# Optimization experiments

Measured on AMD Instinct MI355X. Metric: run time of the kernel, lower is better.

The kernel has to match this reference:

```python
import math
import jax, jax.numpy as jnp
import numpy as np

ALPHA = 0.2                         # LeakyReLU slope
LAMBDA_INIT = 0.8 - 0.6 * math.exp(-0.3 * 1)  # lambda_init_fn(depth=1)
NEG_INF = -9e15
EPS_LN = 1e-5

B, N, IN_F, OUT_F = 4, 2048, 512, 512
INTERNAL = OUT_F // 2
REL_DIM = 10
NUM_REL = 6


def setup_inputs() -> dict:
    key = jax.random.key(0)
    ks = jax.random.split(key, 16)
    xav = lambda k, shape, fan: jax.random.normal(k, shape, jnp.float32) * (1.414 * math.sqrt(2.0 / fan))
    h = jax.random.normal(ks[0], (B, N, IN_F), jnp.float32)
    adj = jax.random.randint(ks[1], (B, N, N), 0, NUM_REL, jnp.int32)
    W = xav(ks[2], (IN_F, OUT_F), IN_F + OUT_F)
    a_left_pos = xav(ks[3], (INTERNAL,), INTERNAL + 1)
    a_right_pos = xav(ks[4], (INTERNAL,), INTERNAL + 1)
    a_left_neg = xav(ks[5], (INTERNAL,), INTERNAL + 1)
    a_right_neg = xav(ks[6], (INTERNAL,), INTERNAL + 1)
    rel_table = jax.random.normal(ks[7], (NUM_REL, REL_DIM), jnp.float32)
    a_rel_pos = xav(ks[8], (REL_DIM,), REL_DIM + 1)
    a_rel_neg = xav(ks[9], (REL_DIM,), REL_DIM + 1)
    ll1 = 0.1 * jax.random.normal(ks[10], (INTERNAL,), jnp.float32)
    lr1 = 0.1 * jax.random.normal(ks[11], (INTERNAL,), jnp.float32)
    ll2 = 0.1 * jax.random.normal(ks[12], (INTERNAL,), jnp.float32)
    lr2 = 0.1 * jax.random.normal(ks[13], (INTERNAL,), jnp.float32)
    ln_gamma = jnp.ones((OUT_F,), jnp.float32)
    ln_beta = jnp.zeros((OUT_F,), jnp.float32)
    return dict(h=h, adj=adj, W=W, a_left_pos=a_left_pos, a_right_pos=a_right_pos,
                a_left_neg=a_left_neg, a_right_neg=a_right_neg, rel_table=rel_table,
                a_rel_pos=a_rel_pos, a_rel_neg=a_rel_neg, ll1=ll1, lr1=lr1,
                ll2=ll2, lr2=lr2, ln_gamma=ln_gamma, ln_beta=ln_beta)


def _leaky(x):
    return jnp.where(x >= 0, x, ALPHA * x)


def reference(h, adj, W, a_left_pos, a_right_pos, a_left_neg, a_right_neg,
              rel_table, a_rel_pos, a_rel_neg, ll1, lr1, ll2, lr2,
              ln_gamma, ln_beta):
    # Projection: Wh [B,N,out] -> split into pos/neg halves [B,N,internal]
    Wh = jnp.einsum('bni,io->bno', h, W)
    Bn, Nn, _ = Wh.shape
    Wh2 = Wh.reshape(Bn, Nn, 2, INTERNAL)
    Wh_pos, Wh_neg = Wh2[:, :, 0, :], Wh2[:, :, 1, :]

    # Additive GAT-style scores: e[b,i,j] = a_left.Wh[i] + a_right.Wh[j]
    e_pos = (Wh_pos @ a_left_pos)[:, :, None] + (Wh_pos @ a_right_pos)[:, None, :]
    e_neg = (Wh_neg @ a_left_neg)[:, :, None] + (Wh_neg @ a_right_neg)[:, None, :]

    # Relation-embedding bias: gather [B,N,N,rel_dim] then project to scalar
    rel_emb = rel_table[adj]                       # [B,N,N,R]
    e_pos = e_pos + rel_emb @ a_rel_pos
    e_neg = e_neg + rel_emb @ a_rel_neg

    mask = adj > 0
    att_pos = jax.nn.softmax(jnp.where(mask, _leaky(e_pos), NEG_INF), axis=2)
    att_neg = jax.nn.softmax(jnp.where(mask, _leaky(e_neg), NEG_INF), axis=2)

    lam = jnp.exp(jnp.sum(ll1 * lr1)) - jnp.exp(jnp.sum(ll2 * lr2)) + LAMBDA_INIT
    attention = att_pos - lam * att_neg            # dropout is identity (eval)

    Wh_v = jnp.concatenate([Wh_pos, Wh_neg], axis=-1)   # [B,N,out]
    h_prime = jnp.einsum('bij,bjd->bid', attention, Wh_v)

    mu = jnp.mean(h_prime, axis=-1, keepdims=True)
    var = jnp.mean(jnp.square(h_prime - mu), axis=-1, keepdims=True)
    h_prime = (h_prime - mu) / jnp.sqrt(var + EPS_LN) * ln_gamma + ln_beta
    h_prime = h_prime * (1 - LAMBDA_INIT)
    return jax.nn.gelu(h_prime, approximate=False), attention
```

## Files before the change

kernel.cpp:

```cpp
#include <hip/hip_runtime.h>
#include <hip/hip_bf16.h>


#define B_ 4
#define N_ 2048
#define F_ 512
#define ALPHA_ 0.2f
#define NEG_INF_ -9000000000000000.0f
#define EPS_LN_ 1e-5f

typedef __attribute__((ext_vector_type(8))) short bf16x8;
typedef __attribute__((ext_vector_type(4))) short bf16x4;
typedef __attribute__((ext_vector_type(4))) float f32x4;

#define HBF_OFF   0
#define WT_OFF    8388608
#define EL_OFF    8912896
#define HP_OFF    0
#define WHT_OFF   16777216
#define ATTBF_OFF 25165824
#define CANON_OFF 58720256
#define SC_OFF    58724352
#define V_OFF     58724416

__device__ __forceinline__ float bf_as_f32(unsigned short u) {
    return __uint_as_float(((unsigned)u) << 16);
}
__device__ __forceinline__ float ldf(const void* p, long i, int isf32) {
    return isf32 ? ((const float*)p)[i] : bf_as_f32(((const unsigned short*)p)[i]);
}
__device__ __forceinline__ short f2bf(float f) {
    __hip_bfloat16 t = __float2bfloat16(f);
    return *reinterpret_cast<short*>(&t);
}
__device__ __forceinline__ int detect_f32(const unsigned short* p) {
    float mx = 0.f;
    for (int i = 0; i < 64; ++i) {
        float x = fabsf(bf_as_f32(p[i]));
        if (x == x && x > mx) mx = x;
    }
    return mx > 1e10f;
}

#define GLL16(g, l) __builtin_amdgcn_global_load_lds( \
    (const __attribute__((address_space(1))) void*)(g), \
    (__attribute__((address_space(3))) void*)(l), 16, 0, 0)

__global__ __launch_bounds__(256) void k_pre(const unsigned short* __restrict__ hraw, const void* __restrict__ W,
                                             const void* alp, const void* arp, const void* aln, const void* arn,
                                             const void* rel, const void* arelp, const void* areln,
                                             const void* ll1, const void* lr1, const void* ll2, const void* lr2,
                                             const void* gam, const void* bet,
                                             __hip_bfloat16* __restrict__ Wt, float* __restrict__ v,
                                             float* __restrict__ canon, float* __restrict__ sc) {
    __shared__ float t[32][33];
    int fl = detect_f32(hraw);
    int bi = blockIdx.x, tid = threadIdx.x, lane = tid & 63, wid = tid >> 6;
    if (bi < 256) {
        int k0 = (bi & 15) * 32, o0 = (bi >> 4) * 32;
        int tx = tid & 31, ty = tid >> 5;
#pragma unroll
        for (int r = 0; r < 4; ++r)
            t[ty + r * 8][tx] = ldf(W, (long)(k0 + ty + r * 8) * 512 + o0 + tx, fl);
        __syncthreads();
#pragma unroll
        for (int r = 0; r < 4; ++r)
            Wt[(o0 + ty + r * 8) * 512 + k0 + tx] = __float2bfloat16(t[tx][ty + r * 8]);
    } else if (bi < 272) {
        int k = (bi - 256) * 32 + (tid >> 3);
        int seg = tid & 7;
        int pos = seg < 4;
        int ob = (seg & 3) * 64 + (pos ? 0 : 256);
        const void* aL = pos ? alp : aln;
        const void* aR = pos ? arp : arn;
        float sL = 0.f, sR = 0.f;
        for (int e = 0; e < 64; ++e) {
            float w = ldf(W, (long)k * 512 + ob + e, fl);
            sL += w * ldf(aL, (ob & 255) + e, fl);
            sR += w * ldf(aR, (ob & 255) + e, fl);
        }
        sL += __shfl_xor(sL, 1); sL += __shfl_xor(sL, 2);
        sR += __shfl_xor(sR, 1); sR += __shfl_xor(sR, 2);
        if ((seg & 3) == 0) {
            int vb = pos ? 0 : 2;
            v[vb * 512 + k] = sL;
            v[(vb + 1) * 512 + k] = sR;
        }
    } else {
        canon[tid] = ldf(gam, tid, fl);
        canon[256 + tid] = ldf(gam, 256 + tid, fl);
        canon[512 + tid] = ldf(bet, tid, fl);
        canon[768 + tid] = ldf(bet, 256 + tid, fl);
        if (wid == 0) {
            float s1 = 0.f, s2 = 0.f;
            for (int k = lane; k < 256; k += 64) {
                s1 += ldf(ll1, k, fl) * ldf(lr1, k, fl);
                s2 += ldf(ll2, k, fl) * ldf(lr2, k, fl);
            }
            for (int off = 32; off; off >>= 1) { s1 += __shfl_down(s1, off); s2 += __shfl_down(s2, off); }
            if (lane == 0) {
                float lam_init = 0.8f - 0.6f * expf(-0.3f);
                sc[0] = expf(s1) - expf(s2) + lam_init;
            }
        } else if (wid == 1 && lane < 6) {
            float p = 0.f, n = 0.f;
            for (int d = 0; d < 10; ++d) {
                float rv = ldf(rel, lane * 10 + d, fl);
                p += rv * ldf(arelp, d, fl);
                n += rv * ldf(areln, d, fl);
            }
            sc[1 + lane] = p;
            sc[7 + lane] = n;
        }
    }
}

__global__ __launch_bounds__(256) void k_conv(const void* __restrict__ h, short* __restrict__ hbf,
                                              const float* __restrict__ v, float* __restrict__ el) {
    int fl = detect_f32((const unsigned short*)h);
    int tid = threadIdx.x, lane = tid & 63;
    long i = ((long)blockIdx.x * 256 + tid) * 8;
    int row = (int)(i >> 9);
    float f[8];
    if (fl) {
        const float4* p = (const float4*)((const float*)h + i);
        float4 a = p[0], b = p[1];
        f[0] = a.x; f[1] = a.y; f[2] = a.z; f[3] = a.w;
        f[4] = b.x; f[5] = b.y; f[6] = b.z; f[7] = b.w;
    } else {
        bf16x8 x = *(const bf16x8*)((const short*)h + i);
#pragma unroll
        for (int e = 0; e < 8; ++e) f[e] = bf_as_f32((unsigned short)x[e]);
    }
    bf16x8 vv;
#pragma unroll
    for (int e = 0; e < 8; ++e) vv[e] = f2bf(f[e]);
    *(bf16x8*)(hbf + i) = vv;
    const float* v0 = v + 0 * 512 + lane * 8;
    const float* v1 = v + 1 * 512 + lane * 8;
    const float* v2 = v + 2 * 512 + lane * 8;
    const float* v3 = v + 3 * 512 + lane * 8;
    float slp = 0.f, srp = 0.f, sln = 0.f, srn = 0.f;
#pragma unroll
    for (int e = 0; e < 8; ++e) {
        slp += f[e] * v0[e]; srp += f[e] * v1[e];
        sln += f[e] * v2[e]; srn += f[e] * v3[e];
    }
    for (int off = 32; off; off >>= 1) {
        slp += __shfl_xor(slp, off); srp += __shfl_xor(srp, off);
        sln += __shfl_xor(sln, off); srn += __shfl_xor(srn, off);
    }
    if (lane == 0) {
        el[row] = slp; el[8192 + row] = srp; el[16384 + row] = sln; el[24576 + row] = srn;
    }
}

template<int TRANS_OUT>
__global__ __launch_bounds__(256) void k_gemm(const short* __restrict__ A, const short* __restrict__ B,
                                              void* __restrict__ Cout, int K, int N,
                                              long aBatch, long bBatch, long cBatch) {
    __shared__ short SM[24576];
    short* As = SM;
    short* Bs = SM + 16384;
    int tid = threadIdx.x, wid = tid >> 6, lane = tid & 63;
    int bm = blockIdx.x * 128, bn = blockIdx.y * 64, bz = blockIdx.z;
    const short* Ab = A + bz * aBatch + (long)bm * K;
    const short* Bb = B + bz * bBatch + (long)bn * K;
    f32x4 acc[4][2] = {};
    int wr = (wid >> 1) * 64, wc = (wid & 1) * 32;
    int l15 = lane & 15, lhi = lane >> 4;
    for (int k0 = 0; k0 < K; k0 += 128) {
        __syncthreads();
#pragma unroll
        for (int j = 0; j < 8; ++j) {
            int q = tid + j * 256;
            int row = q >> 4, c = (q & 15) ^ (row & 7);
            GLL16(Ab + (long)row * K + k0 + c * 8, As + q * 8);
        }
#pragma unroll
        for (int j = 0; j < 4; ++j) {
            int q = tid + j * 256;
            int row = q >> 4, c = (q & 15) ^ (row & 7);
            GLL16(Bb + (long)row * K + k0 + c * 8, Bs + q * 8);
        }
        __syncthreads();
#pragma unroll
        for (int ks = 0; ks < 4; ++ks) {
            bf16x8 af[4], bq[2];
#pragma unroll
            for (int m = 0; m < 4; ++m) {
                int r = wr + m * 16 + l15;
                int c = (ks * 4 + lhi) ^ (r & 7);
                af[m] = *(const bf16x8*)&As[r * 128 + c * 8];
            }
#pragma unroll
            for (int n = 0; n < 2; ++n) {
                int r = wc + n * 16 + l15;
                int c = (ks * 4 + lhi) ^ (r & 7);
                bq[n] = *(const bf16x8*)&Bs[r * 128 + c * 8];
            }
#pragma unroll
            for (int m = 0; m < 4; ++m)
#pragma unroll
                for (int n = 0; n < 2; ++n)
                    acc[m][n] = __builtin_amdgcn_mfma_f32_16x16x32_bf16(af[m], bq[n], acc[m][n], 0, 0, 0);
        }
    }
    int rg = lhi * 4;
    if (TRANS_OUT == 0) {
        float* C = (float*)Cout + bz * cBatch;
#pragma unroll
        for (int m = 0; m < 4; ++m)
#pragma unroll
            for (int n = 0; n < 2; ++n)
#pragma unroll
                for (int r = 0; r < 4; ++r)
                    C[(long)(bm + wr + m * 16 + rg + r) * N + bn + wc + n * 16 + l15] = acc[m][n][r];
    } else {
        __syncthreads();
        short* T = SM;
#pragma unroll
        for (int m = 0; m < 4; ++m)
#pragma unroll
            for (int n = 0; n < 2; ++n) {
                bf16x4 p;
#pragma unroll
                for (int r = 0; r < 4; ++r) p[r] = f2bf(acc[m][n][r]);
                int o = wc + n * 16 + l15;
                int jj = wr + m * 16 + rg;
                *(bf16x4*)&T[o * 136 + jj] = p;
            }
        __syncthreads();
        int b = bm >> 11, jb = bm & 2047;
        int o = tid >> 2, sg = tid & 3;
        short* Wg = (short*)Cout + ((long)b * 512 + bn + o) * 2048 + jb + sg * 32;
#pragma unroll
        for (int w2 = 0; w2 < 4; ++w2)
            *(bf16x8*)(Wg + w2 * 8) = *(bf16x8*)&T[o * 136 + sg * 32 + w2 * 8];
    }
}

__global__ __launch_bounds__(256) void k_attn(const int* __restrict__ adj,
                                              const float* __restrict__ el, const float* __restrict__ sc,
                                              float* __restrict__ att_f32,
                                              __hip_bfloat16* __restrict__ att_bf) {
    __shared__ float s_rp[8], s_rn[8], s_lam[1];
    __shared__ float rmp[4], rmn[4], rsp[4], rsn[4];
    int tid = threadIdx.x, lane = tid & 63, wid = tid >> 6;
    if (tid < 6) { s_rp[tid] = sc[1 + tid]; s_rn[tid] = sc[7 + tid]; }
    if (tid == 6) s_lam[0] = sc[0];
    int m = blockIdx.x, b = m >> 11;
    float elp = el[m], eln = el[16384 + m];
    const float* erp = el + 8192 + b * 2048;
    const float* ern = el + 24576 + b * 2048;
    const int* adjr = adj + (long)m * 2048;
    __syncthreads();
    int j0 = tid * 8;
    int4 A0 = *(const int4*)(adjr + j0), A1 = *(const int4*)(adjr + j0 + 4);
    float4 P0 = *(const float4*)(erp + j0), P1 = *(const float4*)(erp + j0 + 4);
    float4 Q0 = *(const float4*)(ern + j0), Q1 = *(const float4*)(ern + j0 + 4);
    int aa[8] = {A0.x, A0.y, A0.z, A0.w, A1.x, A1.y, A1.z, A1.w};
    float rp[8] = {P0.x, P0.y, P0.z, P0.w, P1.x, P1.y, P1.z, P1.w};
    float rn[8] = {Q0.x, Q0.y, Q0.z, Q0.w, Q1.x, Q1.y, Q1.z, Q1.w};
    float sp[8], sn[8];
    float mp = NEG_INF_, mn = NEG_INF_;
#pragma unroll
    for (int e = 0; e < 8; ++e) {
        int a = aa[e];
        float ep = elp + rp[e] + s_rp[a];
        float en = eln + rn[e] + s_rn[a];
        ep = ep >= 0.f ? ep : ALPHA_ * ep;
        en = en >= 0.f ? en : ALPHA_ * en;
        sp[e] = a > 0 ? ep : NEG_INF_;
        sn[e] = a > 0 ? en : NEG_INF_;
        mp = fmaxf(mp, sp[e]); mn = fmaxf(mn, sn[e]);
    }
    for (int off = 32; off; off >>= 1) { mp = fmaxf(mp, __shfl_down(mp, off)); mn = fmaxf(mn, __shfl_down(mn, off)); }
    if (lane == 0) { rmp[wid] = mp; rmn[wid] = mn; }
    __syncthreads();
    mp = fmaxf(fmaxf(rmp[0], rmp[1]), fmaxf(rmp[2], rmp[3]));
    mn = fmaxf(fmaxf(rmn[0], rmn[1]), fmaxf(rmn[2], rmn[3]));
    float sump = 0.f, sumn = 0.f;
#pragma unroll
    for (int e = 0; e < 8; ++e) {
        sp[e] = __expf(sp[e] - mp);
        sn[e] = __expf(sn[e] - mn);
        sump += sp[e]; sumn += sn[e];
    }
    for (int off = 32; off; off >>= 1) { sump += __shfl_down(sump, off); sumn += __shfl_down(sumn, off); }
    if (lane == 0) { rsp[wid] = sump; rsn[wid] = sumn; }
    __syncthreads();
    sump = rsp[0] + rsp[1] + rsp[2] + rsp[3];
    sumn = rsn[0] + rsn[1] + rsn[2] + rsn[3];
    float ip = 1.0f / sump, inn = 1.0f / sumn;
    float lam = s_lam[0];
    float vout[8];
    bf16x8 vb;
#pragma unroll
    for (int e = 0; e < 8; ++e) {
        vout[e] = sp[e] * ip - lam * sn[e] * inn;
        vb[e] = f2bf(vout[e]);
    }
    float* of = att_f32 + (long)m * 2048 + j0;
    *(float4*)(of)     = make_float4(vout[0], vout[1], vout[2], vout[3]);
    *(float4*)(of + 4) = make_float4(vout[4], vout[5], vout[6], vout[7]);
    *(bf16x8*)((short*)att_bf + (long)m * 2048 + j0) = vb;
}

__global__ __launch_bounds__(256) void k_lngelu(const float* __restrict__ HP, const float* __restrict__ canon,
                                                float* __restrict__ out) {
    int wid = threadIdx.x >> 6, lane = threadIdx.x & 63;
    int m = blockIdx.x * 4 + wid;
    const float* Hr = HP + (long)m * 512 + lane * 8;
    float4 x0 = *(const float4*)(Hr), x1 = *(const float4*)(Hr + 4);
    float x[8] = {x0.x, x0.y, x0.z, x0.w, x1.x, x1.y, x1.z, x1.w};
    float s = 0.f, ss = 0.f;
#pragma unroll
    for (int e = 0; e < 8; ++e) { s += x[e]; ss += x[e] * x[e]; }
    for (int off = 32; off; off >>= 1) { s += __shfl_xor(s, off); ss += __shfl_xor(ss, off); }
    float mu = s * (1.0f / 512.0f);
    float var = ss * (1.0f / 512.0f) - mu * mu;
    float inv = rsqrtf(fmaxf(var, 0.0f) + EPS_LN_);
    float scale = 1.0f - (0.8f - 0.6f * expf(-0.3f));
    const float* g8 = canon + lane * 8;
    const float* b8 = canon + 512 + lane * 8;
    float o[8];
#pragma unroll
    for (int e = 0; e < 8; ++e) {
        float y = (x[e] - mu) * inv * g8[e] + b8[e];
        y *= scale;
        o[e] = 0.5f * y * (1.0f + erff(y * 0.70710678118654752f));
    }
    float* op = out + (long)m * 512 + lane * 8;
    *(float4*)(op)     = make_float4(o[0], o[1], o[2], o[3]);
    *(float4*)(op + 4) = make_float4(o[4], o[5], o[6], o[7]);
}

extern "C" void kernel_launch(void* const* d_in, const int* in_sizes, int n_in,
                              void* d_out, int out_size, void* d_ws, size_t ws_size,
                              hipStream_t stream) {
    const void* h   = d_in[0];
    const int*  adj = (const int*)d_in[1];
    const void* W   = d_in[2];

    char* ws = (char*)d_ws;
    short*          hbf   = (short*)(ws + HBF_OFF);
    __hip_bfloat16* Wt    = (__hip_bfloat16*)(ws + WT_OFF);
    float*          el    = (float*)(ws + EL_OFF);
    float*          HP    = (float*)(ws + HP_OFF);
    __hip_bfloat16* Wht   = (__hip_bfloat16*)(ws + WHT_OFF);
    __hip_bfloat16* attbf = (__hip_bfloat16*)(ws + ATTBF_OFF);
    float*          can   = (float*)(ws + CANON_OFF);
    float*          sc    = (float*)(ws + SC_OFF);
    float*          v     = (float*)(ws + V_OFF);

    float* out_gelu = (float*)d_out;
    float* out_att  = out_gelu + (size_t)B_ * N_ * F_;

    k_pre<<<273, 256, 0, stream>>>((const unsigned short*)h, W,
                                   d_in[3], d_in[4], d_in[5], d_in[6], d_in[7], d_in[8], d_in[9],
                                   d_in[10], d_in[11], d_in[12], d_in[13], d_in[14], d_in[15],
                                   Wt, v, can, sc);
    k_conv<<<2048, 256, 0, stream>>>(h, hbf, v, el);
    k_gemm<1><<<dim3(64, 8, 1), 256, 0, stream>>>(hbf, (const short*)Wt, Wht, 512, 512, 0, 0, 0);
    k_attn<<<8192, 256, 0, stream>>>(adj, el, sc, out_att, attbf);
    k_gemm<0><<<dim3(16, 8, 4), 256, 0, stream>>>((const short*)attbf, (const short*)Wht, HP, 2048, 512,
                                                  2048L * 2048, 512L * 2048, 2048L * 512);
    k_lngelu<<<2048, 256, 0, stream>>>(HP, can, out_gelu);
}
```

Measured before the change: 267.8 us.

## Fuse attention score projections into GEMM epilogue and merge conversion into pre kernel

Removes the separate k_conv kernel. The bf16 conversion of h moves into k_pre as extra blocks, and k_pre now also zeroes el and stores the attention vectors in canon. The left/right score dot products are now computed in the Wh GEMM epilogue from the fp32 accumulators, using shuffle reductions and atomicAdd into el. This drops one kernel launch, one extra pass over h, and the W·a precompute. In exchange it adds atomics and shuffles to the GEMM epilogue, and scores are now built from bf16-rounded h and W products rather than fp32 h.

```diff
diff --git a/kernel.cpp b/kernel.cpp
--- a/kernel.cpp
+++ b/kernel.cpp
@@ -20,8 +20,7 @@
 #define WHT_OFF   16777216
 #define ATTBF_OFF 25165824
 #define CANON_OFF 58720256
-#define SC_OFF    58724352
-#define V_OFF     58724416
+#define SC_OFF    58728448
 
 __device__ __forceinline__ float bf_as_f32(unsigned short u) {
     return __uint_as_float(((unsigned)u) << 16);
@@ -46,18 +45,32 @@
     (const __attribute__((address_space(1))) void*)(g), \
     (__attribute__((address_space(3))) void*)(l), 16, 0, 0)
 
-__global__ __launch_bounds__(256) void k_pre(const unsigned short* __restrict__ hraw, const void* __restrict__ W,
+__global__ __launch_bounds__(256) void k_pre(const void* __restrict__ h, const void* __restrict__ W,
                                              const void* alp, const void* arp, const void* aln, const void* arn,
                                              const void* rel, const void* arelp, const void* areln,
                                              const void* ll1, const void* lr1, const void* ll2, const void* lr2,
                                              const void* gam, const void* bet,
-                                             __hip_bfloat16* __restrict__ Wt, float* __restrict__ v,
-                                             float* __restrict__ canon, float* __restrict__ sc) {
+                                             short* __restrict__ hbf, __hip_bfloat16* __restrict__ Wt,
+                                             float* __restrict__ el, float* __restrict__ canon,
+                                             float* __restrict__ sc) {
     __shared__ float t[32][33];
-    int fl = detect_f32(hraw);
+    int fl = detect_f32((const unsigned short*)h);
     int bi = blockIdx.x, tid = threadIdx.x, lane = tid & 63, wid = tid >> 6;
-    if (bi < 256) {
-        int k0 = (bi & 15) * 32, o0 = (bi >> 4) * 32;
+    if (bi < 2048) {
+        long i = ((long)bi * 256 + tid) * 8;
+        bf16x8 vv;
+        if (fl) {
+            const float4* p = (const float4*)((const float*)h + i);
+            float4 a = p[0], b = p[1];
+            vv[0] = f2bf(a.x); vv[1] = f2bf(a.y); vv[2] = f2bf(a.z); vv[3] = f2bf(a.w);
+            vv[4] = f2bf(b.x); vv[5] = f2bf(b.y); vv[6] = f2bf(b.z); vv[7] = f2bf(b.w);
+        } else {
+            vv = *(const bf16x8*)((const short*)h + i);
+        }
+        *(bf16x8*)(hbf + i) = vv;
+    } else if (bi < 2304) {
+        int b2 = bi - 2048;
+        int k0 = (b2 & 15) * 32, o0 = (b2 >> 4) * 32;
         int tx = tid & 31, ty = tid >> 5;
 #pragma unroll
         for (int r = 0; r < 4; ++r)
@@ -66,31 +79,20 @@
 #pragma unroll
         for (int r = 0; r < 4; ++r)
             Wt[(o0 + ty + r * 8) * 512 + k0 + tx] = __float2bfloat16(t[tx][ty + r * 8]);
-    } else if (bi < 272) {
-        int k = (bi - 256) * 32 + (tid >> 3);
-        int seg = tid & 7;
-        int pos = seg < 4;
-        int ob = (seg & 3) * 64 + (pos ? 0 : 256);
-        const void* aL = pos ? alp : aln;
-        const void* aR = pos ? arp : arn;
-        float sL = 0.f, sR = 0.f;
-        for (int e = 0; e < 64; ++e) {
-            float w = ldf(W, (long)k * 512 + ob + e, fl);
-            sL += w * ldf(aL, (ob & 255) + e, fl);
-            sR += w * ldf(aR, (ob & 255) + e, fl);
-        }
-        sL += __shfl_xor(sL, 1); sL += __shfl_xor(sL, 2);
-        sR += __shfl_xor(sR, 1); sR += __shfl_xor(sR, 2);
-        if ((seg & 3) == 0) {
-            int vb = pos ? 0 : 2;
-            v[vb * 512 + k] = sL;
-            v[(vb + 1) * 512 + k] = sR;
-        }
+    } else if (bi < 2320) {
+        int base = (bi - 2304) * 2048 + tid * 8;
+        float4 z = make_float4(0.f, 0.f, 0.f, 0.f);
+        *(float4*)(el + base) = z;
+        *(float4*)(el + base + 4) = z;
     } else {
         canon[tid] = ldf(gam, tid, fl);
         canon[256 + tid] = ldf(gam, 256 + tid, fl);
         canon[512 + tid] = ldf(bet, tid, fl);
         canon[768 + tid] = ldf(bet, 256 + tid, fl);
+        canon[1024 + tid] = ldf(alp, tid, fl);
+        canon[1280 + tid] = ldf(arp, tid, fl);
+        canon[1536 + tid] = ldf(aln, tid, fl);
+        canon[1792 + tid] = ldf(arn, tid, fl);
         if (wid == 0) {
             float s1 = 0.f, s2 = 0.f;
             for (int k = lane; k < 256; k += 64) {
@@ -115,50 +117,11 @@
     }
 }
 
-__global__ __launch_bounds__(256) void k_conv(const void* __restrict__ h, short* __restrict__ hbf,
-                                              const float* __restrict__ v, float* __restrict__ el) {
-    int fl = detect_f32((const unsigned short*)h);
-    int tid = threadIdx.x, lane = tid & 63;
-    long i = ((long)blockIdx.x * 256 + tid) * 8;
-    int row = (int)(i >> 9);
-    float f[8];
-    if (fl) {
-        const float4* p = (const float4*)((const float*)h + i);
-        float4 a = p[0], b = p[1];
-        f[0] = a.x; f[1] = a.y; f[2] = a.z; f[3] = a.w;
-        f[4] = b.x; f[5] = b.y; f[6] = b.z; f[7] = b.w;
-    } else {
-        bf16x8 x = *(const bf16x8*)((const short*)h + i);
-#pragma unroll
-        for (int e = 0; e < 8; ++e) f[e] = bf_as_f32((unsigned short)x[e]);
-    }
-    bf16x8 vv;
-#pragma unroll
-    for (int e = 0; e < 8; ++e) vv[e] = f2bf(f[e]);
-    *(bf16x8*)(hbf + i) = vv;
-    const float* v0 = v + 0 * 512 + lane * 8;
-    const float* v1 = v + 1 * 512 + lane * 8;
-    const float* v2 = v + 2 * 512 + lane * 8;
-    const float* v3 = v + 3 * 512 + lane * 8;
-    float slp = 0.f, srp = 0.f, sln = 0.f, srn = 0.f;
-#pragma unroll
-    for (int e = 0; e < 8; ++e) {
-        slp += f[e] * v0[e]; srp += f[e] * v1[e];
-        sln += f[e] * v2[e]; srn += f[e] * v3[e];
-    }
-    for (int off = 32; off; off >>= 1) {
-        slp += __shfl_xor(slp, off); srp += __shfl_xor(srp, off);
-        sln += __shfl_xor(sln, off); srn += __shfl_xor(srn, off);
-    }
-    if (lane == 0) {
-        el[row] = slp; el[8192 + row] = srp; el[16384 + row] = sln; el[24576 + row] = srn;
-    }
-}
-
 template<int TRANS_OUT>
 __global__ __launch_bounds__(256) void k_gemm(const short* __restrict__ A, const short* __restrict__ B,
                                               void* __restrict__ Cout, int K, int N,
-                                              long aBatch, long bBatch, long cBatch) {
+                                              long aBatch, long bBatch, long cBatch,
+                                              const float* __restrict__ canon, float* __restrict__ el) {
     __shared__ short SM[24576];
     short* As = SM;
     short* Bs = SM + 16384;
@@ -217,6 +180,32 @@
                 for (int r = 0; r < 4; ++r)
                     C[(long)(bm + wr + m * 16 + rg + r) * N + bn + wc + n * 16 + l15] = acc[m][n][r];
     } else {
+        int pos = bn < 256;
+        int obase = (pos ? bn : bn - 256) + wc;
+        const float* aL = canon + (pos ? 1024 : 1536);
+        const float* aR = aL + 256;
+        float aLv[2], aRv[2];
+#pragma unroll
+        for (int n = 0; n < 2; ++n) {
+            int ol = obase + n * 16 + l15;
+            aLv[n] = aL[ol]; aRv[n] = aR[ol];
+        }
+#pragma unroll
+        for (int m = 0; m < 4; ++m)
+#pragma unroll
+            for (int r = 0; r < 4; ++r) {
+                float sL = acc[m][0][r] * aLv[0] + acc[m][1][r] * aLv[1];
+                float sR = acc[m][0][r] * aRv[0] + acc[m][1][r] * aRv[1];
+#pragma unroll
+                for (int off = 1; off < 16; off <<= 1) {
+                    sL += __shfl_xor(sL, off); sR += __shfl_xor(sR, off);
+                }
+                if (l15 == 0) {
+                    int rowg = bm + wr + m * 16 + rg + r;
+                    atomicAdd(&el[(pos ? 0 : 2) * 8192 + rowg], sL);
+                    atomicAdd(&el[(pos ? 1 : 3) * 8192 + rowg], sR);
+                }
+            }
         __syncthreads();
         short* T = SM;
 #pragma unroll
@@ -352,19 +341,17 @@
     __hip_bfloat16* attbf = (__hip_bfloat16*)(ws + ATTBF_OFF);
     float*          can   = (float*)(ws + CANON_OFF);
     float*          sc    = (float*)(ws + SC_OFF);
-    float*          v     = (float*)(ws + V_OFF);
 
     float* out_gelu = (float*)d_out;
     float* out_att  = out_gelu + (size_t)B_ * N_ * F_;
 
-    k_pre<<<273, 256, 0, stream>>>((const unsigned short*)h, W,
-                                   d_in[3], d_in[4], d_in[5], d_in[6], d_in[7], d_in[8], d_in[9],
-                                   d_in[10], d_in[11], d_in[12], d_in[13], d_in[14], d_in[15],
-                                   Wt, v, can, sc);
-    k_conv<<<2048, 256, 0, stream>>>(h, hbf, v, el);
-    k_gemm<1><<<dim3(64, 8, 1), 256, 0, stream>>>(hbf, (const short*)Wt, Wht, 512, 512, 0, 0, 0);
+    k_pre<<<2321, 256, 0, stream>>>(h, W,
+                                    d_in[3], d_in[4], d_in[5], d_in[6], d_in[7], d_in[8], d_in[9],
+                                    d_in[10], d_in[11], d_in[12], d_in[13], d_in[14], d_in[15],
+                                    hbf, Wt, el, can, sc);
+    k_gemm<1><<<dim3(64, 8, 1), 256, 0, stream>>>(hbf, (const short*)Wt, Wht, 512, 512, 0, 0, 0, can, el);
     k_attn<<<8192, 256, 0, stream>>>(adj, el, sc, out_att, attbf);
     k_gemm<0><<<dim3(16, 8, 4), 256, 0, stream>>>((const short*)attbf, (const short*)Wht, HP, 2048, 512,
-                                                  2048L * 2048, 512L * 2048, 2048L * 512);
+                                                  2048L * 2048, 512L * 2048, 2048L * 512, can, el);
     k_lngelu<<<2048, 256, 0, stream>>>(HP, can, out_gelu);
 }
```

Result: faster. 257.2 us (-4.0%).
